# Performance work log

Measured on AMD Instinct MI355X. Metric: run time of the kernel, lower is better.

## Reference

```python
import jax, jax.numpy as jnp
import numpy as np

N = 8192
IN_F, OUT_F = 256, 128
N_REL = 2


def setup_inputs() -> dict:
    key = jax.random.key(0)
    ks = jax.random.split(key, 7)
    std0 = 1.0 / np.sqrt(OUT_F)
    return {
        "x_feature": jax.random.normal(ks[0], (N, IN_F), dtype=jnp.float32),
        "all_adj_matrix": jax.random.uniform(ks[1], (N, N, N_REL), dtype=jnp.float32),
        "w0": jax.random.uniform(ks[2], (IN_F, OUT_F), minval=-std0, maxval=std0, dtype=jnp.float32),
        "b0": jax.random.uniform(ks[3], (OUT_F,), minval=-std0, maxval=std0, dtype=jnp.float32),
        "w1": jax.random.uniform(ks[4], (OUT_F, OUT_F), minval=-std0, maxval=std0, dtype=jnp.float32),
        "b1": jax.random.uniform(ks[5], (OUT_F,), minval=-std0, maxval=std0, dtype=jnp.float32),
        "relation_weight": jax.random.uniform(ks[6], (N_REL, 1), minval=0.0, maxval=0.1, dtype=jnp.float32),
    }


def reference(x_feature, all_adj_matrix, w0, b0, w1, b1, relation_weight):
    # combine relations: [N,N,R] @ [R,1] -> [N,N], then symmetrize
    adj = jnp.einsum('ijr,rk->ij', all_adj_matrix, relation_weight)
    adj = adj + adj.T
    # layer 1: dense transform then aggregation
    h1 = adj @ (x_feature @ w0) + b0            # [N, OUT_F]
    # layer 2
    h2 = adj @ (h1 @ w1) + b1                   # [N, OUT_F]
    # mean over the two layer outputs
    return 0.5 * (h1 + h2)
```

## Files before the change

### kernel.cpp

```cpp
#include <hip/hip_runtime.h>
#include <stdint.h>


#define NN 8192
#define KIN 256
#define FOUT 128
#define SPLITK 8
#define KCHUNK (NN / SPLITK)
#define LDP 40

typedef __bf16 bf16x8 __attribute__((ext_vector_type(8)));
typedef float f32x4 __attribute__((ext_vector_type(4)));
typedef uint16_t u16x8 __attribute__((ext_vector_type(8)));

__device__ __forceinline__ float bf2f(uint16_t u) {
    union { uint32_t u; float f; } c; c.u = ((uint32_t)u) << 16; return c.f;
}
__device__ __forceinline__ uint16_t f2bf(float f) {
    union { float f; uint32_t u; } c; c.f = f;
    uint32_t r = c.u + 0x7fffu + ((c.u >> 16) & 1u);
    return (uint16_t)(r >> 16);
}
__device__ __forceinline__ float combineAt(const void* adj, size_t idx,
                                           bool isbf, float r0, float r1) {
    if (isbf) {
        uint32_t u = ((const uint32_t*)adj)[idx];
        return bf2f((uint16_t)(u & 0xffffu)) * r0 + bf2f((uint16_t)(u >> 16)) * r1;
    } else {
        float2 v = ((const float2*)adj)[idx];
        return v.x * r0 + v.y * r1;
    }
}

__global__ __launch_bounds__(256) void probe_kernel(
        const uint16_t* __restrict__ xr, int* __restrict__ flag) {
    __shared__ int cnt;
    if (threadIdx.x == 0) cnt = 0;
    __syncthreads();
    uint16_t v = xr[threadIdx.x * 16];
    int e = (v >> 7) & 0xFF;
    if (e >= 96 && e <= 144) atomicAdd(&cnt, 1);
    __syncthreads();
    if (threadIdx.x == 0) flag[0] = (cnt >= 128) ? 1 : 0;
}

__global__ __launch_bounds__(256) void init_bias_kernel(
        const void* __restrict__ b0p, const void* __restrict__ b1p,
        float* __restrict__ h1, float* __restrict__ h2,
        const int* __restrict__ flag) {
    bool isbf = flag[0] != 0;
    int idx = (blockIdx.x * 256 + threadIdx.x) * 4;
    int f = idx & (FOUT - 1);
    float4 v0, v1;
    if (isbf) {
        const uint16_t* b0 = (const uint16_t*)b0p;
        const uint16_t* b1 = (const uint16_t*)b1p;
        v0 = make_float4(bf2f(b0[f]), bf2f(b0[f+1]), bf2f(b0[f+2]), bf2f(b0[f+3]));
        v1 = make_float4(bf2f(b1[f]), bf2f(b1[f+1]), bf2f(b1[f+2]), bf2f(b1[f+3]));
    } else {
        v0 = *(const float4*)((const float*)b0p + f);
        v1 = *(const float4*)((const float*)b1p + f);
    }
    *(float4*)(h1 + idx) = v0;
    *(float4*)(h2 + idx) = v1;
}

__global__ __launch_bounds__(256) void xw0_kernel(
        const void* __restrict__ xp, const void* __restrict__ w0p,
        uint16_t* __restrict__ xw0T, const int* __restrict__ flag) {
    bool isbf = flag[0] != 0;
    int t = blockIdx.x * 256 + threadIdx.x;
    int j = t >> 4;
    int f0 = (t & 15) * 8;
    float acc[8] = {0.f,0.f,0.f,0.f,0.f,0.f,0.f,0.f};
    if (isbf) {
        const uint16_t* xrow = (const uint16_t*)xp + (size_t)j * KIN;
        const uint16_t* w0 = (const uint16_t*)w0p;
        for (int k8 = 0; k8 < KIN; k8 += 8) {
            u16x8 xv = *(const u16x8*)(xrow + k8);
            #pragma unroll
            for (int i = 0; i < 8; i++) {
                float a = bf2f(xv[i]);
                u16x8 wv = *(const u16x8*)(w0 + (size_t)(k8 + i) * FOUT + f0);
                #pragma unroll
                for (int q = 0; q < 8; q++) acc[q] += a * bf2f(wv[q]);
            }
        }
    } else {
        const float* xrow = (const float*)xp + (size_t)j * KIN;
        const float* w0 = (const float*)w0p;
        for (int k4 = 0; k4 < KIN; k4 += 4) {
            float4 xv = *(const float4*)(xrow + k4);
            float xa[4] = {xv.x, xv.y, xv.z, xv.w};
            #pragma unroll
            for (int i = 0; i < 4; i++) {
                const float* wr = w0 + (size_t)(k4 + i) * FOUT + f0;
                float4 wa = *(const float4*)wr;
                float4 wb = *(const float4*)(wr + 4);
                acc[0] += xa[i]*wa.x; acc[1] += xa[i]*wa.y;
                acc[2] += xa[i]*wa.z; acc[3] += xa[i]*wa.w;
                acc[4] += xa[i]*wb.x; acc[5] += xa[i]*wb.y;
                acc[6] += xa[i]*wb.z; acc[7] += xa[i]*wb.w;
            }
        }
    }
    #pragma unroll
    for (int q = 0; q < 8; q++) xw0T[(size_t)(f0 + q) * NN + j] = f2bf(acc[q]);
}

__global__ __launch_bounds__(256) void sym_kernel(
        const void* __restrict__ adj, const void* __restrict__ rwp,
        uint16_t* __restrict__ sym, const int* __restrict__ flag) {
    int I = blockIdx.x, J = blockIdx.y;
    if (J < I) return;
    bool isbf = flag[0] != 0;
    float r0 = isbf ? bf2f(((const uint16_t*)rwp)[0]) : ((const float*)rwp)[0];
    float r1 = isbf ? bf2f(((const uint16_t*)rwp)[1]) : ((const float*)rwp)[1];
    __shared__ float Ds[64][65];
    __shared__ float Es[64][65];
    int i0 = I * 64, j0 = J * 64;
    int t = threadIdx.x;
    #pragma unroll
    for (int s = 0; s < 16; s++) {
        int q = s * 256 + t;
        int a = q >> 6, b = q & 63;
        Ds[a][b] = combineAt(adj, (size_t)(i0 + a) * NN + (j0 + b), isbf, r0, r1);
        Es[a][b] = combineAt(adj, (size_t)(j0 + a) * NN + (i0 + b), isbf, r0, r1);
    }
    __syncthreads();
    if (I == J) {
        #pragma unroll
        for (int s = 0; s < 16; s++) {
            int q = s * 256 + t;
            int a = q >> 6, b = q & 63;
            sym[(size_t)(i0 + a) * NN + (j0 + b)] = f2bf(Ds[a][b] + Es[b][a]);
        }
    } else {
        #pragma unroll
        for (int s = 0; s < 16; s++) {
            int q = s * 256 + t;
            int a = q >> 6, b = q & 63;
            sym[(size_t)(i0 + a) * NN + (j0 + b)] = f2bf(Ds[a][b] + Es[b][a]);
            sym[(size_t)(j0 + a) * NN + (i0 + b)] = f2bf(Es[a][b] + Ds[b][a]);
        }
    }
}

__global__ __launch_bounds__(256) void gemm_atomic_kernel(
        const uint16_t* __restrict__ A, const uint16_t* __restrict__ BT,
        float* __restrict__ out) {
    __shared__ __align__(16) uint16_t As[128 * LDP];
    __shared__ __align__(16) uint16_t Bs[128 * LDP];
    const int m0 = blockIdx.x * 128;
    const int k0 = blockIdx.y * KCHUNK;
    const int t = threadIdx.x;
    const int w = t >> 6;
    const int L = t & 63;
    const int mb = (w & 1) * 64;
    const int nb = (w >> 1) * 64;
    const int fr_l = L & 15;
    const int fr_k = (L >> 4) * 8;
    const int sr = t >> 2;
    const int sk = (t & 3) * 8;

    f32x4 acc[4][4];
    #pragma unroll
    for (int r = 0; r < 4; r++)
        #pragma unroll
        for (int c = 0; c < 4; c++)
            acc[r][c] = (f32x4){0.f, 0.f, 0.f, 0.f};

    for (int kk = 0; kk < KCHUNK; kk += 32) {
        const int kg = k0 + kk;
        uint4 av0 = *(const uint4*)(A + (size_t)(m0 + sr) * NN + kg + sk);
        uint4 av1 = *(const uint4*)(A + (size_t)(m0 + 64 + sr) * NN + kg + sk);
        uint4 bv0 = *(const uint4*)(BT + (size_t)sr * NN + kg + sk);
        uint4 bv1 = *(const uint4*)(BT + (size_t)(64 + sr) * NN + kg + sk);
        __syncthreads();
        *(uint4*)(As + sr * LDP + sk) = av0;
        *(uint4*)(As + (64 + sr) * LDP + sk) = av1;
        *(uint4*)(Bs + sr * LDP + sk) = bv0;
        *(uint4*)(Bs + (64 + sr) * LDP + sk) = bv1;
        __syncthreads();

        bf16x8 af[4], bf[4];
        #pragma unroll
        for (int r = 0; r < 4; r++)
            af[r] = *(const bf16x8*)(As + (mb + r * 16 + fr_l) * LDP + fr_k);
        #pragma unroll
        for (int c = 0; c < 4; c++)
            bf[c] = *(const bf16x8*)(Bs + (nb + c * 16 + fr_l) * LDP + fr_k);
        #pragma unroll
        for (int r = 0; r < 4; r++)
            #pragma unroll
            for (int c = 0; c < 4; c++)
                acc[r][c] = __builtin_amdgcn_mfma_f32_16x16x32_bf16(af[r], bf[c], acc[r][c], 0, 0, 0);
    }

    #pragma unroll
    for (int r = 0; r < 4; r++)
        #pragma unroll
        for (int c = 0; c < 4; c++) {
            int col = nb + c * 16 + (L & 15);
            int rowb = m0 + mb + r * 16 + (L >> 4) * 4;
            #pragma unroll
            for (int q = 0; q < 4; q++)
                atomicAdd(out + (size_t)(rowb + q) * FOUT + col, acc[r][c][q]);
        }
}

__global__ __launch_bounds__(256) void gemm_otf_kernel(
        const void* __restrict__ adj, const uint16_t* __restrict__ BT,
        float* __restrict__ out, const void* __restrict__ rwp,
        const int* __restrict__ flag) {
    bool isbf = flag[0] != 0;
    float r0 = isbf ? bf2f(((const uint16_t*)rwp)[0]) : ((const float*)rwp)[0];
    float r1 = isbf ? bf2f(((const uint16_t*)rwp)[1]) : ((const float*)rwp)[1];
    __shared__ __align__(16) uint16_t As[128 * LDP];
    __shared__ __align__(16) uint16_t Bs[128 * LDP];
    const int m0 = blockIdx.x * 128;
    const int k0 = blockIdx.y * KCHUNK;
    const int t = threadIdx.x;
    const int w = t >> 6;
    const int L = t & 63;
    const int mb = (w & 1) * 64;
    const int nb = (w >> 1) * 64;
    const int fr_l = L & 15;
    const int fr_k = (L >> 4) * 8;
    const int sr = t >> 2;
    const int sk = (t & 3) * 8;

    f32x4 acc[4][4];
    #pragma unroll
    for (int r = 0; r < 4; r++)
        #pragma unroll
        for (int c = 0; c < 4; c++)
            acc[r][c] = (f32x4){0.f, 0.f, 0.f, 0.f};

    for (int kk = 0; kk < KCHUNK; kk += 32) {
        const int kg = k0 + kk;
        uint4 bv0 = *(const uint4*)(BT + (size_t)sr * NN + kg + sk);
        uint4 bv1 = *(const uint4*)(BT + (size_t)(64 + sr) * NN + kg + sk);
        __syncthreads();
        *(uint4*)(Bs + sr * LDP + sk) = bv0;
        *(uint4*)(Bs + (64 + sr) * LDP + sk) = bv1;
        #pragma unroll
        for (int s = 0; s < 16; s++) {
            int idx = s * 256 + t;
            int m = idx >> 5, k = idx & 31;
            As[m * LDP + k] = f2bf(combineAt(adj, (size_t)(m0 + m) * NN + (kg + k), isbf, r0, r1));
        }
        __syncthreads();
        #pragma unroll
        for (int s = 0; s < 16; s++) {
            int idx = s * 256 + t;
            int k = idx >> 7, m = idx & 127;
            float v2 = combineAt(adj, (size_t)(kg + k) * NN + (m0 + m), isbf, r0, r1);
            As[m * LDP + k] = f2bf(bf2f(As[m * LDP + k]) + v2);
        }
        __syncthreads();

        bf16x8 af[4], bf[4];
        #pragma unroll
        for (int r = 0; r < 4; r++)
            af[r] = *(const bf16x8*)(As + (mb + r * 16 + fr_l) * LDP + fr_k);
        #pragma unroll
        for (int c = 0; c < 4; c++)
            bf[c] = *(const bf16x8*)(Bs + (nb + c * 16 + fr_l) * LDP + fr_k);
        #pragma unroll
        for (int r = 0; r < 4; r++)
            #pragma unroll
            for (int c = 0; c < 4; c++)
                acc[r][c] = __builtin_amdgcn_mfma_f32_16x16x32_bf16(af[r], bf[c], acc[r][c], 0, 0, 0);
    }

    #pragma unroll
    for (int r = 0; r < 4; r++)
        #pragma unroll
        for (int c = 0; c < 4; c++) {
            int col = nb + c * 16 + (L & 15);
            int rowb = m0 + mb + r * 16 + (L >> 4) * 4;
            #pragma unroll
            for (int q = 0; q < 4; q++)
                atomicAdd(out + (size_t)(rowb + q) * FOUT + col, acc[r][c][q]);
        }
}

__global__ __launch_bounds__(256) void h1w1_kernel(
        const float* __restrict__ h1, const void* __restrict__ w1p,
        uint16_t* __restrict__ hwT, const int* __restrict__ flag) {
    bool isbf = flag[0] != 0;
    int t = blockIdx.x * 256 + threadIdx.x;
    int j = t >> 4;
    int f0 = (t & 15) * 8;
    float acc[8] = {0.f,0.f,0.f,0.f,0.f,0.f,0.f,0.f};
    const float* hrow = h1 + (size_t)j * FOUT;
    if (isbf) {
        const uint16_t* w1 = (const uint16_t*)w1p;
        for (int k4 = 0; k4 < FOUT; k4 += 4) {
            float4 a4 = *(const float4*)(hrow + k4);
            float av[4] = {a4.x, a4.y, a4.z, a4.w};
            #pragma unroll
            for (int i = 0; i < 4; i++) {
                u16x8 wv = *(const u16x8*)(w1 + (size_t)(k4 + i) * FOUT + f0);
                #pragma unroll
                for (int q = 0; q < 8; q++) acc[q] += av[i] * bf2f(wv[q]);
            }
        }
    } else {
        const float* w1 = (const float*)w1p;
        for (int k4 = 0; k4 < FOUT; k4 += 4) {
            float4 a4 = *(const float4*)(hrow + k4);
            float av[4] = {a4.x, a4.y, a4.z, a4.w};
            #pragma unroll
            for (int i = 0; i < 4; i++) {
                const float* wr = w1 + (size_t)(k4 + i) * FOUT + f0;
                float4 wa = *(const float4*)wr;
                float4 wb = *(const float4*)(wr + 4);
                acc[0] += av[i]*wa.x; acc[1] += av[i]*wa.y;
                acc[2] += av[i]*wa.z; acc[3] += av[i]*wa.w;
                acc[4] += av[i]*wb.x; acc[5] += av[i]*wb.y;
                acc[6] += av[i]*wb.z; acc[7] += av[i]*wb.w;
            }
        }
    }
    #pragma unroll
    for (int q = 0; q < 8; q++) hwT[(size_t)(f0 + q) * NN + j] = f2bf(acc[q]);
}

__global__ __launch_bounds__(256) void final_kernel(
        const float* __restrict__ h1, const float* __restrict__ h2,
        void* __restrict__ outp, const int* __restrict__ flag) {
    int idx = (blockIdx.x * 256 + threadIdx.x) * 4;
    float4 a = *(const float4*)(h1 + idx);
    float4 b = *(const float4*)(h2 + idx);
    float4 r = make_float4(0.5f*(a.x+b.x), 0.5f*(a.y+b.y), 0.5f*(a.z+b.z), 0.5f*(a.w+b.w));
    if (flag[0] != 0) {
        ushort4 ov = make_ushort4(f2bf(r.x), f2bf(r.y), f2bf(r.z), f2bf(r.w));
        *(ushort4*)((uint16_t*)outp + idx) = ov;
    } else {
        *(float4*)((float*)outp + idx) = r;
    }
}

extern "C" void kernel_launch(void* const* d_in, const int* in_sizes, int n_in,
                              void* d_out, int out_size, void* d_ws, size_t ws_size,
                              hipStream_t stream) {
    char* ws = (char*)d_ws;
    uint16_t* xw0T = (uint16_t*)(ws);
    uint16_t* hwT  = (uint16_t*)(ws + (2u << 20));
    float*    h1   = (float*)   (ws + (4u << 20));
    float*    h2   = (float*)   (ws + (8u << 20));
    int*      flag = (int*)     (ws + (12u << 20));
    uint16_t* sym  = (uint16_t*)(ws + (13u << 20));
    const size_t need_fast = ((size_t)13 << 20) + (size_t)NN * NN * 2;
    const bool fast = ws_size >= need_fast;

    probe_kernel<<<1, 256, 0, stream>>>((const uint16_t*)d_in[0], flag);
    init_bias_kernel<<<1024, 256, 0, stream>>>(d_in[3], d_in[5], h1, h2, flag);
    xw0_kernel<<<512, 256, 0, stream>>>(d_in[0], d_in[2], xw0T, flag);
    if (fast) {
        sym_kernel<<<dim3(128, 128), 256, 0, stream>>>(d_in[1], d_in[6], sym, flag);
        gemm_atomic_kernel<<<dim3(64, SPLITK), 256, 0, stream>>>(sym, xw0T, h1);
    } else {
        gemm_otf_kernel<<<dim3(64, SPLITK), 256, 0, stream>>>(d_in[1], xw0T, h1, d_in[6], flag);
    }
    h1w1_kernel<<<512, 256, 0, stream>>>(h1, d_in[4], hwT, flag);
    if (fast) {
        gemm_atomic_kernel<<<dim3(64, SPLITK), 256, 0, stream>>>(sym, hwT, h2);
    } else {
        gemm_otf_kernel<<<dim3(64, SPLITK), 256, 0, stream>>>(d_in[1], hwT, h2, d_in[6], flag);
    }
    final_kernel<<<1024, 256, 0, stream>>>(h1, h2, d_out, flag);
}
```

Measured before the change: 983.5 us.

## Replace split-K atomics with partial buffers and fused reductions; vectorize sym kernel

The split-K GEMMs now write per-split partial tiles to a workspace buffer instead of issuing float atomics. Separate reduce kernels sum them, with bias add, h1@w1 and the final averaging fused in, which drops the init_bias, h1w1 and final kernels on the fast path. The symmetrize kernel now uses wider vector loads and stores. This needs a larger workspace (176 MiB) to take the fast path, and it adds extra partial-buffer traffic.

```diff
diff --git a/kernel.cpp b/kernel.cpp
--- a/kernel.cpp
+++ b/kernel.cpp
@@ -29,6 +29,18 @@
     } else {
         float2 v = ((const float2*)adj)[idx];
         return v.x * r0 + v.y * r1;
+    }
+}
+__device__ __forceinline__ float2 combine2At(const void* adj, size_t idx,
+                                             bool isbf, float r0, float r1) {
+    if (isbf) {
+        uint2 u = ((const uint2*)adj)[idx >> 1];
+        return make_float2(
+            bf2f((uint16_t)(u.x & 0xffffu)) * r0 + bf2f((uint16_t)(u.x >> 16)) * r1,
+            bf2f((uint16_t)(u.y & 0xffffu)) * r0 + bf2f((uint16_t)(u.y >> 16)) * r1);
+    } else {
+        float4 v = ((const float4*)adj)[idx >> 1];
+        return make_float2(v.x * r0 + v.y * r1, v.z * r0 + v.w * r1);
     }
 }
 
@@ -121,34 +133,39 @@
     int i0 = I * 64, j0 = J * 64;
     int t = threadIdx.x;
     #pragma unroll
-    for (int s = 0; s < 16; s++) {
+    for (int s = 0; s < 8; s++) {
         int q = s * 256 + t;
-        int a = q >> 6, b = q & 63;
-        Ds[a][b] = combineAt(adj, (size_t)(i0 + a) * NN + (j0 + b), isbf, r0, r1);
-        Es[a][b] = combineAt(adj, (size_t)(j0 + a) * NN + (i0 + b), isbf, r0, r1);
+        int a = q >> 5, b2 = (q & 31) * 2;
+        float2 d = combine2At(adj, (size_t)(i0 + a) * NN + (j0 + b2), isbf, r0, r1);
+        Ds[a][b2] = d.x; Ds[a][b2 + 1] = d.y;
+        float2 e = combine2At(adj, (size_t)(j0 + a) * NN + (i0 + b2), isbf, r0, r1);
+        Es[a][b2] = e.x; Es[a][b2 + 1] = e.y;
     }
     __syncthreads();
-    if (I == J) {
-        #pragma unroll
-        for (int s = 0; s < 16; s++) {
-            int q = s * 256 + t;
-            int a = q >> 6, b = q & 63;
-            sym[(size_t)(i0 + a) * NN + (j0 + b)] = f2bf(Ds[a][b] + Es[b][a]);
-        }
-    } else {
-        #pragma unroll
-        for (int s = 0; s < 16; s++) {
-            int q = s * 256 + t;
-            int a = q >> 6, b = q & 63;
-            sym[(size_t)(i0 + a) * NN + (j0 + b)] = f2bf(Ds[a][b] + Es[b][a]);
-            sym[(size_t)(j0 + a) * NN + (i0 + b)] = f2bf(Es[a][b] + Ds[b][a]);
-        }
-    }
-}
-
-__global__ __launch_bounds__(256) void gemm_atomic_kernel(
+    #pragma unroll
+    for (int s = 0; s < 4; s++) {
+        int q = s * 256 + t;
+        int a = q >> 4, b4 = (q & 15) * 4;
+        ushort4 o;
+        o.x = f2bf(Ds[a][b4 + 0] + Es[b4 + 0][a]);
+        o.y = f2bf(Ds[a][b4 + 1] + Es[b4 + 1][a]);
+        o.z = f2bf(Ds[a][b4 + 2] + Es[b4 + 2][a]);
+        o.w = f2bf(Ds[a][b4 + 3] + Es[b4 + 3][a]);
+        *(ushort4*)(sym + (size_t)(i0 + a) * NN + (j0 + b4)) = o;
+        if (I != J) {
+            ushort4 p4;
+            p4.x = f2bf(Es[a][b4 + 0] + Ds[b4 + 0][a]);
+            p4.y = f2bf(Es[a][b4 + 1] + Ds[b4 + 1][a]);
+            p4.z = f2bf(Es[a][b4 + 2] + Ds[b4 + 2][a]);
+            p4.w = f2bf(Es[a][b4 + 3] + Ds[b4 + 3][a]);
+            *(ushort4*)(sym + (size_t)(j0 + a) * NN + (i0 + b4)) = p4;
+        }
+    }
+}
+
+__global__ __launch_bounds__(256) void gemm_part_kernel(
         const uint16_t* __restrict__ A, const uint16_t* __restrict__ BT,
-        float* __restrict__ out) {
+        float* __restrict__ P) {
     __shared__ __align__(16) uint16_t As[128 * LDP];
     __shared__ __align__(16) uint16_t Bs[128 * LDP];
     const int m0 = blockIdx.x * 128;
@@ -197,6 +214,7 @@
                 acc[r][c] = __builtin_amdgcn_mfma_f32_16x16x32_bf16(af[r], bf[c], acc[r][c], 0, 0, 0);
     }
 
+    float* part = P + (size_t)blockIdx.y * NN * FOUT;
     #pragma unroll
     for (int r = 0; r < 4; r++)
         #pragma unroll
@@ -205,7 +223,7 @@
             int rowb = m0 + mb + r * 16 + (L >> 4) * 4;
             #pragma unroll
             for (int q = 0; q < 4; q++)
-                atomicAdd(out + (size_t)(rowb + q) * FOUT + col, acc[r][c][q]);
+                part[(size_t)(rowb + q) * FOUT + col] = acc[r][c][q];
         }
 }
 
@@ -286,6 +304,96 @@
         }
 }
 
+__global__ __launch_bounds__(256) void reduce1_kernel(
+        const float* __restrict__ P, const void* __restrict__ b0p,
+        const void* __restrict__ w1p, float* __restrict__ h1,
+        uint16_t* __restrict__ hwT, const int* __restrict__ flag) {
+    bool isbf = flag[0] != 0;
+    __shared__ float hs[16][132];
+    const int t = threadIdx.x;
+    const int jr = t >> 4;
+    const int f0 = (t & 15) * 8;
+    const int j = blockIdx.x * 16 + jr;
+    f32x4 s0 = (f32x4){0.f,0.f,0.f,0.f}, s1 = (f32x4){0.f,0.f,0.f,0.f};
+    const float* Pj = P + (size_t)j * FOUT + f0;
+    #pragma unroll
+    for (int p = 0; p < SPLITK; p++) {
+        const float* pp = Pj + (size_t)p * NN * FOUT;
+        s0 += *(const f32x4*)pp;
+        s1 += *(const f32x4*)(pp + 4);
+    }
+    if (isbf) {
+        const uint16_t* b0 = (const uint16_t*)b0p;
+        #pragma unroll
+        for (int q = 0; q < 4; q++) { s0[q] += bf2f(b0[f0+q]); s1[q] += bf2f(b0[f0+4+q]); }
+    } else {
+        const float* b0 = (const float*)b0p;
+        s0 += *(const f32x4*)(b0 + f0);
+        s1 += *(const f32x4*)(b0 + f0 + 4);
+    }
+    *(f32x4*)(h1 + (size_t)j * FOUT + f0) = s0;
+    *(f32x4*)(h1 + (size_t)j * FOUT + f0 + 4) = s1;
+    *(f32x4*)(&hs[jr][f0]) = s0;
+    *(f32x4*)(&hs[jr][f0 + 4]) = s1;
+    __syncthreads();
+    float acc[8] = {0.f,0.f,0.f,0.f,0.f,0.f,0.f,0.f};
+    if (isbf) {
+        const uint16_t* w1 = (const uint16_t*)w1p;
+        for (int k4 = 0; k4 < FOUT; k4 += 4) {
+            f32x4 a4 = *(const f32x4*)(&hs[jr][k4]);
+            #pragma unroll
+            for (int i = 0; i < 4; i++) {
+                u16x8 wv = *(const u16x8*)(w1 + (size_t)(k4 + i) * FOUT + f0);
+                #pragma unroll
+                for (int q = 0; q < 8; q++) acc[q] += a4[i] * bf2f(wv[q]);
+            }
+        }
+    } else {
+        const float* w1 = (const float*)w1p;
+        for (int k4 = 0; k4 < FOUT; k4 += 4) {
+            f32x4 a4 = *(const f32x4*)(&hs[jr][k4]);
+            #pragma unroll
+            for (int i = 0; i < 4; i++) {
+                const float* wr = w1 + (size_t)(k4 + i) * FOUT + f0;
+                f32x4 wa = *(const f32x4*)wr;
+                f32x4 wb = *(const f32x4*)(wr + 4);
+                #pragma unroll
+                for (int q = 0; q < 4; q++) { acc[q] += a4[i]*wa[q]; acc[4+q] += a4[i]*wb[q]; }
+            }
+        }
+    }
+    #pragma unroll
+    for (int q = 0; q < 8; q++) hwT[(size_t)(f0 + q) * NN + j] = f2bf(acc[q]);
+}
+
+__global__ __launch_bounds__(256) void reduce2_kernel(
+        const float* __restrict__ P, const void* __restrict__ b1p,
+        const float* __restrict__ h1, void* __restrict__ outp,
+        const int* __restrict__ flag) {
+    bool isbf = flag[0] != 0;
+    int idx = (blockIdx.x * 256 + threadIdx.x) * 4;
+    int f = idx & (FOUT - 1);
+    f32x4 s = (f32x4){0.f,0.f,0.f,0.f};
+    #pragma unroll
+    for (int p = 0; p < SPLITK; p++)
+        s += *(const f32x4*)(P + (size_t)p * NN * FOUT + idx);
+    if (isbf) {
+        const uint16_t* b1 = (const uint16_t*)b1p;
+        #pragma unroll
+        for (int q = 0; q < 4; q++) s[q] += bf2f(b1[f + q]);
+    } else {
+        s += *(const f32x4*)((const float*)b1p + f);
+    }
+    f32x4 h = *(const f32x4*)(h1 + idx);
+    f32x4 r = 0.5f * (h + s);
+    if (isbf) {
+        ushort4 ov = make_ushort4(f2bf(r[0]), f2bf(r[1]), f2bf(r[2]), f2bf(r[3]));
+        *(ushort4*)((uint16_t*)outp + idx) = ov;
+    } else {
+        *(f32x4*)((float*)outp + idx) = r;
+    }
+}
+
 __global__ __launch_bounds__(256) void h1w1_kernel(
         const float* __restrict__ h1, const void* __restrict__ w1p,
         uint16_t* __restrict__ hwT, const int* __restrict__ flag) {
@@ -353,23 +461,23 @@
     float*    h2   = (float*)   (ws + (8u << 20));
     int*      flag = (int*)     (ws + (12u << 20));
     uint16_t* sym  = (uint16_t*)(ws + (13u << 20));
-    const size_t need_fast = ((size_t)13 << 20) + (size_t)NN * NN * 2;
+    float*    P    = (float*)   (ws + ((size_t)144 << 20));
+    const size_t need_fast = (size_t)176 << 20;
     const bool fast = ws_size >= need_fast;
 
     probe_kernel<<<1, 256, 0, stream>>>((const uint16_t*)d_in[0], flag);
-    init_bias_kernel<<<1024, 256, 0, stream>>>(d_in[3], d_in[5], h1, h2, flag);
     xw0_kernel<<<512, 256, 0, stream>>>(d_in[0], d_in[2], xw0T, flag);
     if (fast) {
         sym_kernel<<<dim3(128, 128), 256, 0, stream>>>(d_in[1], d_in[6], sym, flag);
-        gemm_atomic_kernel<<<dim3(64, SPLITK), 256, 0, stream>>>(sym, xw0T, h1);
-    } else {
+        gemm_part_kernel<<<dim3(64, SPLITK), 256, 0, stream>>>(sym, xw0T, P);
+        reduce1_kernel<<<512, 256, 0, stream>>>(P, d_in[3], d_in[4], h1, hwT, flag);
+        gemm_part_kernel<<<dim3(64, SPLITK), 256, 0, stream>>>(sym, hwT, P);
+        reduce2_kernel<<<1024, 256, 0, stream>>>(P, d_in[5], h1, d_out, flag);
+    } else {
+        init_bias_kernel<<<1024, 256, 0, stream>>>(d_in[3], d_in[5], h1, h2, flag);
         gemm_otf_kernel<<<dim3(64, SPLITK), 256, 0, stream>>>(d_in[1], xw0T, h1, d_in[6], flag);
-    }
-    h1w1_kernel<<<512, 256, 0, stream>>>(h1, d_in[4], hwT, flag);
-    if (fast) {
-        gemm_atomic_kernel<<<dim3(64, SPLITK), 256, 0, stream>>>(sym, hwT, h2);
-    } else {
+        h1w1_kernel<<<512, 256, 0, stream>>>(h1, d_in[4], hwT, flag);
         gemm_otf_kernel<<<dim3(64, SPLITK), 256, 0, stream>>>(d_in[1], hwT, h2, d_in[6], flag);
-    }
-    final_kernel<<<1024, 256, 0, stream>>>(h1, h2, d_out, flag);
-}
+        final_kernel<<<1024, 256, 0, stream>>>(h1, h2, d_out, flag);
+    }
+}
```

Result: faster. 896.3 us (-8.9%).
